# Optimization experiments

Measured on AMD Instinct MI355X. Metric: run time of the kernel, lower is better.

The kernel has to match this reference:

```python
import jax, jax.numpy as jnp
import numpy as np

L, D, H, DFF, A, S = 8, 1024, 16, 4096, 4096, 66
T = S + 1  # 67 after pool token
DK = D // H
EPS = 1e-5


def _pos_enc(t, d):
    pos = np.arange(t, dtype=np.float32)[:, None]
    div = np.exp(np.arange(0, d, 2, dtype=np.float32) * (-np.log(10000.0) / d))
    pe = np.zeros((t, d), dtype=np.float32)
    pe[:, 0::2] = np.sin(pos * div)
    pe[:, 1::2] = np.cos(pos * div)
    return jnp.asarray(pe)


def _ln(x, g, b):
    m = jnp.mean(x, axis=-1, keepdims=True)
    v = jnp.mean(jnp.square(x - m), axis=-1, keepdims=True)
    return (x - m) * jax.lax.rsqrt(v + EPS) * g + b


def setup_inputs() -> dict:
    key = jax.random.key(0)
    ks = jax.random.split(key, 12)
    B = 256
    sc = 0.02
    return {
        "x": jax.random.randint(ks[0], (B, S), 0, A, dtype=jnp.int32),
        "emb": jax.random.normal(ks[1], (A, D), jnp.float32) * sc,
        "pool": jax.random.normal(ks[2], (D,), jnp.float32) * sc,
        "Wq": jax.random.normal(ks[3], (L, D, D), jnp.float32) * sc,
        "Wk": jax.random.normal(ks[4], (L, D, D), jnp.float32) * sc,
        "Wv": jax.random.normal(ks[5], (L, D, D), jnp.float32) * sc,
        "Wo": jax.random.normal(ks[6], (L, D, D), jnp.float32) * sc,
        "rel_bias": jax.random.normal(ks[7], (L, H, 78, 78), jnp.float32) * sc,
        "ln1_g": jnp.ones((L, D), jnp.float32),
        "ln1_b": jnp.zeros((L, D), jnp.float32),
        "ln2_g": jnp.ones((L, D), jnp.float32),
        "ln2_b": jnp.zeros((L, D), jnp.float32),
        "W1": jax.random.normal(ks[8], (L, D, DFF), jnp.float32) * sc,
        "b1": jnp.zeros((L, DFF), jnp.float32),
        "W2": jax.random.normal(ks[9], (L, DFF, D), jnp.float32) * sc,
        "b2": jnp.zeros((L, D), jnp.float32),
        "Wout": jax.random.normal(ks[10], (D, A), jnp.float32) * sc,
        "bout": jnp.zeros((A,), jnp.float32),
    }


def reference(x, emb, pool, Wq, Wk, Wv, Wo, rel_bias, ln1_g, ln1_b, ln2_g, ln2_b,
              W1, b1, W2, b2, Wout, bout):
    B = x.shape[0]
    h = emb[x] * jnp.sqrt(jnp.float32(D))            # (B, S, D)
    h = jnp.concatenate([jnp.broadcast_to(pool, (B, 1, D)), h], axis=1)  # (B, T, D)
    h = h + _pos_enc(T, D)[None]
    scale = 1.0 / jnp.sqrt(jnp.float32(DK))
    for i in range(L):
        q = (h @ Wq[i]).reshape(B, T, H, DK)
        k = (h @ Wk[i]).reshape(B, T, H, DK)
        v = (h @ Wv[i]).reshape(B, T, H, DK)
        scores = jnp.einsum("bqhd,bkhd->bhqk", q, k) * scale + rel_bias[i][:, :T, :T]
        attn = jax.nn.softmax(scores, axis=-1)
        ctx = jnp.einsum("bhqk,bkhd->bqhd", attn, v).reshape(B, T, D)
        h = _ln(h + ctx @ Wo[i], ln1_g[i], ln1_b[i])
        f = jax.nn.gelu(h @ W1[i] + b1[i], approximate=False) @ W2[i] + b2[i]
        h = _ln(h + f, ln2_g[i], ln2_b[i])
    return h[:, 0, :] @ Wout + bout  # (B, A)
```

## Files before the change

### kernel.cpp

```cpp
#include <hip/hip_runtime.h>
#include <math.h>

typedef unsigned short u16;
typedef __attribute__((ext_vector_type(8))) short short8;
typedef __attribute__((ext_vector_type(4))) float f32x4;

#define LAYERS 8
#define D 1024
#define NH 16
#define DKH 64
#define DFF 4096
#define SEQ 66
#define TT 67
#define BATCH 256
#define ROWS (BATCH*TT)
#define VOCAB 4096
#define TP 80
#define KP 96
#define QS 3072

__device__ __forceinline__ float bf2f(u16 v){
  unsigned int u = ((unsigned int)v) << 16;
  return __builtin_bit_cast(float, u);
}
__device__ __forceinline__ u16 f2bf(float f){
  unsigned int u = __builtin_bit_cast(unsigned int, f);
  u += 0x7FFFu + ((u >> 16) & 1u);
  return (u16)(u >> 16);
}
__device__ __forceinline__ void gload16(const u16* g, u16* l){
  __builtin_amdgcn_global_load_lds((const __attribute__((address_space(1))) void*)g,
                                   (__attribute__((address_space(3))) void*)l, 16, 0, 0);
}

__global__ void transpose_cast(const float* __restrict__ src, u16* __restrict__ dst,
                               int R, int C){
  __shared__ float tile[32][33];
  const int c0 = blockIdx.x * 32, r0 = blockIdx.y * 32;
  const int tx = threadIdx.x, ty = threadIdx.y;
  #pragma unroll
  for (int i = 0; i < 32; i += 8)
    tile[ty + i][tx] = src[(size_t)(r0 + ty + i) * C + (c0 + tx)];
  __syncthreads();
  #pragma unroll
  for (int i = 0; i < 32; i += 8)
    dst[(size_t)(c0 + ty + i) * R + (r0 + tx)] = f2bf(tile[tx][ty + i]);
}

__global__ void embed_kernel(const int* __restrict__ x, const float* __restrict__ emb,
                             const float* __restrict__ pool, float* __restrict__ h,
                             u16* __restrict__ hb){
  const int row = blockIdx.x;
  const int b = row / TT, t = row % TT;
  const int d0 = threadIdx.x * 4;
  float v[4];
  if (t == 0){
    const float4 p4 = *(const float4*)&pool[d0];
    v[0] = p4.x; v[1] = p4.y; v[2] = p4.z; v[3] = p4.w;
  } else {
    const int id = x[b * SEQ + (t - 1)];
    const float4 e4 = *(const float4*)&emb[(size_t)id * D + d0];
    v[0] = e4.x * 32.f; v[1] = e4.y * 32.f; v[2] = e4.z * 32.f; v[3] = e4.w * 32.f;
  }
  const float c = -logf(10000.f) / (float)D;
  float o[4];
  #pragma unroll
  for (int j = 0; j < 4; j++){
    const int d = d0 + j;
    const int p = d >> 1;
    const float freq = expf((float)(2 * p) * c);
    const float ang = (float)t * freq;
    const float pe = (d & 1) ? cosf(ang) : sinf(ang);
    o[j] = v[j] + pe;
  }
  *(float4*)&h[(size_t)row * D + d0] = make_float4(o[0], o[1], o[2], o[3]);
  const unsigned int lo = (unsigned)f2bf(o[0]) | ((unsigned)f2bf(o[1]) << 16);
  const unsigned int hi = (unsigned)f2bf(o[2]) | ((unsigned)f2bf(o[3]) << 16);
  *(uint2*)&hb[(size_t)row * D + d0] = make_uint2(lo, hi);
}

__global__ void ln_kernel(float* __restrict__ h, const float* __restrict__ res,
                          u16* __restrict__ hb, const float* __restrict__ g,
                          const float* __restrict__ bta){
  const int row = blockIdx.x;
  const int tid = threadIdx.x;
  const size_t off = (size_t)row * D + tid * 4;
  const float4 a = *(const float4*)&h[off];
  const float4 r4 = *(const float4*)&res[off];
  const float s0 = a.x + r4.x, s1 = a.y + r4.y, s2 = a.z + r4.z, s3 = a.w + r4.w;
  float sum = s0 + s1 + s2 + s3;
  float sq = s0*s0 + s1*s1 + s2*s2 + s3*s3;
  #pragma unroll
  for (int m = 32; m >= 1; m >>= 1){ sum += __shfl_xor(sum, m); sq += __shfl_xor(sq, m); }
  __shared__ float red[2][4];
  const int w = tid >> 6;
  if ((tid & 63) == 0){ red[0][w] = sum; red[1][w] = sq; }
  __syncthreads();
  sum = red[0][0] + red[0][1] + red[0][2] + red[0][3];
  sq  = red[1][0] + red[1][1] + red[1][2] + red[1][3];
  const float mean = sum * (1.f / D);
  const float var = sq * (1.f / D) - mean * mean;
  const float rs = rsqrtf(var + 1e-5f);
  const float4 gv = *(const float4*)&g[tid * 4];
  const float4 bv = *(const float4*)&bta[tid * 4];
  const float o0 = (s0 - mean) * rs * gv.x + bv.x;
  const float o1 = (s1 - mean) * rs * gv.y + bv.y;
  const float o2 = (s2 - mean) * rs * gv.z + bv.z;
  const float o3 = (s3 - mean) * rs * gv.w + bv.w;
  *(float4*)&h[off] = make_float4(o0, o1, o2, o3);
  const unsigned int lo = (unsigned)f2bf(o0) | ((unsigned)f2bf(o1) << 16);
  const unsigned int hi = (unsigned)f2bf(o2) | ((unsigned)f2bf(o3) << 16);
  *(uint2*)&hb[off] = make_uint2(lo, hi);
}

__global__ __launch_bounds__(256) void attn_kernel(const u16* __restrict__ qkv,
    const float* __restrict__ rel, u16* __restrict__ ctxb){
  __shared__ u16 Qf[8 * 81 * 8];
  __shared__ u16 Kf[8 * 81 * 8];
  __shared__ u16 Vf[12 * 65 * 8];
  __shared__ u16 Pf[12 * 81 * 8];
  __shared__ float Ss[TP][84];
  const int bh = blockIdx.x;
  const int b = bh >> 4, hh = bh & 15;
  const int tid = threadIdx.x, w = tid >> 6, l = tid & 63;
  const size_t qvbase = (size_t)(b * TT) * QS + hh * DKH;
  const size_t obase  = (size_t)(b * TT) * D + hh * DKH;

  {
    const int r0 = tid >> 4, c4 = (tid & 15) * 4;
    const int g = c4 >> 3, e = c4 & 7;
    for (int r = r0; r < TP; r += 16){
      uint2 q2 = make_uint2(0u, 0u), k2 = make_uint2(0u, 0u);
      if (r < TT){
        q2 = *(const uint2*)&qkv[qvbase + (size_t)r * QS + c4];
        k2 = *(const uint2*)&qkv[qvbase + 1024 + (size_t)r * QS + c4];
      }
      *(uint2*)&Qf[(g * 81 + r) * 8 + e] = q2;
      *(uint2*)&Kf[(g * 81 + r) * 8 + e] = k2;
    }
    for (int j = r0; j < KP; j += 16){
      u16 v4[4] = {0, 0, 0, 0};
      if (j < TT) *(uint2*)v4 = *(const uint2*)&qkv[qvbase + 2048 + (size_t)j * QS + c4];
      const int gg = j >> 3, ee = j & 7;
      #pragma unroll
      for (int d = 0; d < 4; d++)
        Vf[(gg * 65 + (c4 + d)) * 8 + ee] = v4[d];
    }
  }
  __syncthreads();

  const int fr = l & 15, gg = l >> 4;
  for (int p = w; p < 25; p += 4){
    const int rt = p / 5, ct = p % 5;
    f32x4 acc = {};
    #pragma unroll
    for (int kk = 0; kk < 2; kk++){
      const short8 a  = *(const short8*)&Qf[((kk * 4 + gg) * 81 + rt * 16 + fr) * 8];
      const short8 bf = *(const short8*)&Kf[((kk * 4 + gg) * 81 + ct * 16 + fr) * 8];
      acc = __builtin_amdgcn_mfma_f32_16x16x32_bf16(a, bf, acc, 0, 0, 0);
    }
    const int col = ct * 16 + fr;
    #pragma unroll
    for (int r = 0; r < 4; r++){
      const int row = rt * 16 + gg * 4 + r;
      float sv = -1e30f;
      if (row < TT && col < TT)
        sv = acc[r] * 0.125f + rel[((size_t)hh * 78 + row) * 78 + col];
      Ss[row][col] = sv;
    }
  }
  __syncthreads();

  for (int row = w; row < TP; row += 4){
    const float s1 = Ss[row][l];
    const float s2 = (l < 16) ? Ss[row][64 + l] : -1e30f;
    float mx = fmaxf(s1, s2);
    #pragma unroll
    for (int m = 32; m >= 1; m >>= 1) mx = fmaxf(mx, __shfl_xor(mx, m));
    const float e1 = __expf(s1 - mx);
    const float e2 = (l < 16) ? __expf(s2 - mx) : 0.f;
    float sum = e1 + e2;
    #pragma unroll
    for (int m = 32; m >= 1; m >>= 1) sum += __shfl_xor(sum, m);
    const float inv = 1.f / sum;
    Pf[((l >> 3) * 81 + row) * 8 + (l & 7)] = f2bf(e1 * inv);
    if (l < 16){
      Pf[((8  + (l >> 3)) * 81 + row) * 8 + (l & 7)] = f2bf(e2 * inv);
      Pf[((10 + (l >> 3)) * 81 + row) * 8 + (l & 7)] = 0;
    }
  }
  __syncthreads();

  for (int p = w; p < 20; p += 4){
    const int rt = p >> 2, ct = p & 3;
    f32x4 acc = {};
    #pragma unroll
    for (int kk = 0; kk < 3; kk++){
      const short8 a  = *(const short8*)&Pf[((kk * 4 + gg) * 81 + rt * 16 + fr) * 8];
      const short8 bf = *(const short8*)&Vf[((kk * 4 + gg) * 65 + ct * 16 + fr) * 8];
      acc = __builtin_amdgcn_mfma_f32_16x16x32_bf16(a, bf, acc, 0, 0, 0);
    }
    #pragma unroll
    for (int r = 0; r < 4; r++){
      const int row = rt * 16 + gg * 4 + r;
      if (row < TT)
        ctxb[obase + (size_t)row * D + ct * 16 + fr] = f2bf(acc[r]);
    }
  }
}

template<int OBF16, int BIAS, int GELU>
__global__ __launch_bounds__(256, 2) void gemm_bt(
    const u16* __restrict__ A, int lda,
    const u16* __restrict__ Bt,
    void* __restrict__ Cv, int ldc,
    const float* __restrict__ bias, int K, int nby)
{
  __shared__ u16 As[128 * 32];
  __shared__ u16 Bs[128 * 32];
  const int nwg = gridDim.x, bid = blockIdx.x;
  const int q8 = nwg >> 3, r8 = nwg & 7;
  const int xcd = bid & 7, off = bid >> 3;
  const int wg = (xcd < r8 ? xcd * (q8 + 1) : r8 * (q8 + 1) + (xcd - r8) * q8) + off;
  const int m0 = (wg / nby) * 128, n0 = (wg % nby) * 128;

  const int tid = threadIdx.x;
  const int l = tid & 63, w = tid >> 6;
  const int wr = w >> 1, wc = w & 1;
  f32x4 acc[4][4] = {};
  const int lr = l >> 2;
  const int lseg = (l & 3) * 8;
  u16* aB0 = &As[(w * 32) * 32];
  u16* aB1 = &As[(w * 32 + 16) * 32];
  u16* bB0 = &Bs[(w * 32) * 32];
  u16* bB1 = &Bs[(w * 32 + 16) * 32];
  const u16* ga0 = A + (size_t)(m0 + w * 32 + lr) * lda + lseg;
  const u16* ga1 = A + (size_t)(m0 + w * 32 + 16 + lr) * lda + lseg;
  const u16* gb0 = Bt + (size_t)(n0 + w * 32 + lr) * K + lseg;
  const u16* gb1 = Bt + (size_t)(n0 + w * 32 + 16 + lr) * K + lseg;
  const int fr = l & 15, kg = (l >> 4) * 8;
  for (int kt = 0; kt < K; kt += 32){
    __syncthreads();
    gload16(ga0 + kt, aB0);
    gload16(ga1 + kt, aB1);
    gload16(gb0 + kt, bB0);
    gload16(gb1 + kt, bB1);
    __syncthreads();
    short8 af[4], bf[4];
    #pragma unroll
    for (int i = 0; i < 4; i++){
      af[i] = *(const short8*)&As[(wr * 64 + i * 16 + fr) * 32 + kg];
      bf[i] = *(const short8*)&Bs[(wc * 64 + i * 16 + fr) * 32 + kg];
    }
    #pragma unroll
    for (int i = 0; i < 4; i++)
      #pragma unroll
      for (int j = 0; j < 4; j++)
        acc[i][j] = __builtin_amdgcn_mfma_f32_16x16x32_bf16(af[i], bf[j], acc[i][j], 0, 0, 0);
  }
  const int rg = (l >> 4) * 4;
  #pragma unroll
  for (int i = 0; i < 4; i++){
    #pragma unroll
    for (int j = 0; j < 4; j++){
      const int col = n0 + wc * 64 + j * 16 + fr;
      const float bv = BIAS ? bias[col] : 0.f;
      #pragma unroll
      for (int r = 0; r < 4; r++){
        const int row = m0 + wr * 64 + i * 16 + rg + r;
        float xv = acc[i][j][r] + bv;
        if (GELU) xv = 0.5f * xv * (1.f + erff(xv * 0.70710678118f));
        if (OBF16) ((u16*)Cv)[(size_t)row * ldc + col] = f2bf(xv);
        else       ((float*)Cv)[(size_t)row * ldc + col] = xv;
      }
    }
  }
}

extern "C" void kernel_launch(void* const* d_in, const int* in_sizes, int n_in,
                              void* d_out, int out_size, void* d_ws, size_t ws_size,
                              hipStream_t stream) {
  const int*   x       = (const int*)  d_in[0];
  const float* emb     = (const float*)d_in[1];
  const float* pool    = (const float*)d_in[2];
  const float* Wq      = (const float*)d_in[3];
  const float* Wk      = (const float*)d_in[4];
  const float* Wv      = (const float*)d_in[5];
  const float* Wo      = (const float*)d_in[6];
  const float* rel     = (const float*)d_in[7];
  const float* ln1_g   = (const float*)d_in[8];
  const float* ln1_b   = (const float*)d_in[9];
  const float* ln2_g   = (const float*)d_in[10];
  const float* ln2_b   = (const float*)d_in[11];
  const float* W1      = (const float*)d_in[12];
  const float* b1      = (const float*)d_in[13];
  const float* W2      = (const float*)d_in[14];
  const float* b2      = (const float*)d_in[15];
  const float* Wout    = (const float*)d_in[16];
  const float* bout    = (const float*)d_in[17];
  float* out = (float*)d_out;

  const size_t SZ_WDD  = (size_t)D * D * 2;
  const size_t SZ_WDF  = (size_t)D * DFF * 2;
  const size_t SZ_H    = (size_t)ROWS * D * 4;
  const size_t SZ_HB   = (size_t)ROWS * D * 2;
  const size_t need = 4*SZ_WDD + 3*SZ_WDF + SZ_H + SZ_HB + 4*SZ_HB + SZ_H;
  if (ws_size < need) return;

  char* p = (char*)d_ws;
  u16* WqkvT = (u16*)p; p += 3*SZ_WDD;
  u16* WoT   = (u16*)p; p += SZ_WDD;
  u16* W1T   = (u16*)p; p += SZ_WDF;
  u16* W2T   = (u16*)p; p += SZ_WDF;
  u16* WouT  = (u16*)p; p += SZ_WDF;
  float* h   = (float*)p; p += SZ_H;
  u16* hb    = (u16*)p; p += SZ_HB;
  u16* qkv   = (u16*)p; p += 3*SZ_HB;
  u16* ctxb  = (u16*)p; p += SZ_HB;
  u16* gb    = qkv;
  float* tmp = (float*)p; p += SZ_H;

  dim3 tb(32, 8);
  transpose_cast<<<dim3(VOCAB/32, D/32), tb, 0, stream>>>(Wout, WouT, D, VOCAB);
  embed_kernel<<<ROWS, 256, 0, stream>>>(x, emb, pool, h, hb);

  const int MB = ROWS / 128;
  for (int l = 0; l < LAYERS; ++l){
    const size_t wo = (size_t)l * D * D;
    const size_t wf = (size_t)l * D * DFF;
    transpose_cast<<<dim3(D/32,   D/32),   tb, 0, stream>>>(Wq + wo, WqkvT,         D, D);
    transpose_cast<<<dim3(D/32,   D/32),   tb, 0, stream>>>(Wk + wo, WqkvT + D*D,   D, D);
    transpose_cast<<<dim3(D/32,   D/32),   tb, 0, stream>>>(Wv + wo, WqkvT + 2*D*D, D, D);
    transpose_cast<<<dim3(D/32,   D/32),   tb, 0, stream>>>(Wo + wo, WoT, D, D);
    transpose_cast<<<dim3(DFF/32, D/32),   tb, 0, stream>>>(W1 + wf, W1T, D, DFF);
    transpose_cast<<<dim3(D/32,   DFF/32), tb, 0, stream>>>(W2 + wf, W2T, DFF, D);

    gemm_bt<1,0,0><<<MB * (QS/128),  256, 0, stream>>>(hb, D, WqkvT, qkv, QS, nullptr, D, QS/128);
    attn_kernel<<<BATCH*NH, 256, 0, stream>>>(qkv, rel + (size_t)l*NH*78*78, ctxb);
    gemm_bt<0,0,0><<<MB * (D/128),   256, 0, stream>>>(ctxb, D, WoT, tmp, D, nullptr, D, D/128);
    ln_kernel<<<ROWS, 256, 0, stream>>>(h, tmp, hb, ln1_g + l*D, ln1_b + l*D);
    gemm_bt<1,1,1><<<MB * (DFF/128), 256, 0, stream>>>(hb, D, W1T, gb, DFF, b1 + l*DFF, D, DFF/128);
    gemm_bt<0,1,0><<<MB * (D/128),   256, 0, stream>>>(gb, DFF, W2T, tmp, D, b2 + l*D, DFF, D/128);
    ln_kernel<<<ROWS, 256, 0, stream>>>(h, tmp, hb, ln2_g + l*D, ln2_b + l*D);
  }
  gemm_bt<0,1,0><<<(BATCH/128) * (VOCAB/128), 256, 0, stream>>>(
      hb, TT * D, WouT, out, VOCAB, bout, D, VOCAB/128);
}
```

Baseline: 7.013 ms.

## Double-buffer GEMM LDS tiles, merge weight transposes, store residual in bf16

The GEMM now keeps two LDS buffers and issues the global-to-LDS loads for the next K tile before running the MFMAs on the current one, so there is one barrier per iteration instead of two and load latency can overlap compute. The six per-layer weight transpose launches are merged into a single kernel. The Wo and W2 GEMM outputs feeding layer norm are written as bf16 instead of fp32, which halves that traffic but loses some precision in the residual add. Doubling LDS per block may limit occupancy.

Measured after the change: 6.656 ms. 1.05x faster.

```diff
diff --git a/kernel.cpp b/kernel.cpp
--- a/kernel.cpp
+++ b/kernel.cpp
@@ -33,18 +33,43 @@
                                    (__attribute__((address_space(3))) void*)l, 16, 0, 0);
 }
 
+__device__ __forceinline__ void tc_tile(const float* __restrict__ src, u16* __restrict__ dst,
+                                        int R, int C, int bx, int by, int tx, int ty){
+  __shared__ float tile[32][33];
+  const int c0 = bx * 32, r0 = by * 32;
+  #pragma unroll
+  for (int i = 0; i < 32; i += 8)
+    tile[ty + i][tx] = src[(size_t)(r0 + ty + i) * C + (c0 + tx)];
+  __syncthreads();
+  #pragma unroll
+  for (int i = 0; i < 32; i += 8)
+    dst[(size_t)(c0 + ty + i) * R + (r0 + tx)] = f2bf(tile[tx][ty + i]);
+}
+
+__global__ void transpose6(const float* __restrict__ Wq, const float* __restrict__ Wk,
+                           const float* __restrict__ Wv, const float* __restrict__ Wo,
+                           const float* __restrict__ W1, const float* __restrict__ W2,
+                           u16* __restrict__ WqkvT, u16* __restrict__ WoT,
+                           u16* __restrict__ W1T, u16* __restrict__ W2T){
+  const int tx = threadIdx.x, ty = threadIdx.y;
+  int b = blockIdx.x;
+  if (b < 4096){
+    const int which = b >> 10, idx = b & 1023;
+    const float* s = which == 0 ? Wq : which == 1 ? Wk : which == 2 ? Wv : Wo;
+    u16* d = which == 3 ? WoT : WqkvT + which * D * D;
+    tc_tile(s, d, D, D, idx & 31, idx >> 5, tx, ty);
+  } else if (b < 8192){
+    const int idx = b - 4096;
+    tc_tile(W1, W1T, D, DFF, idx & 127, idx >> 7, tx, ty);
+  } else {
+    const int idx = b - 8192;
+    tc_tile(W2, W2T, DFF, D, idx & 31, idx >> 5, tx, ty);
+  }
+}
+
 __global__ void transpose_cast(const float* __restrict__ src, u16* __restrict__ dst,
                                int R, int C){
-  __shared__ float tile[32][33];
-  const int c0 = blockIdx.x * 32, r0 = blockIdx.y * 32;
-  const int tx = threadIdx.x, ty = threadIdx.y;
-  #pragma unroll
-  for (int i = 0; i < 32; i += 8)
-    tile[ty + i][tx] = src[(size_t)(r0 + ty + i) * C + (c0 + tx)];
-  __syncthreads();
-  #pragma unroll
-  for (int i = 0; i < 32; i += 8)
-    dst[(size_t)(c0 + ty + i) * R + (r0 + tx)] = f2bf(tile[tx][ty + i]);
+  tc_tile(src, dst, R, C, blockIdx.x, blockIdx.y, threadIdx.x, threadIdx.y);
 }
 
 __global__ void embed_kernel(const int* __restrict__ x, const float* __restrict__ emb,
@@ -79,15 +104,18 @@
   *(uint2*)&hb[(size_t)row * D + d0] = make_uint2(lo, hi);
 }
 
-__global__ void ln_kernel(float* __restrict__ h, const float* __restrict__ res,
+__global__ void ln_kernel(float* __restrict__ h, const u16* __restrict__ res,
                           u16* __restrict__ hb, const float* __restrict__ g,
                           const float* __restrict__ bta){
   const int row = blockIdx.x;
   const int tid = threadIdx.x;
   const size_t off = (size_t)row * D + tid * 4;
   const float4 a = *(const float4*)&h[off];
-  const float4 r4 = *(const float4*)&res[off];
-  const float s0 = a.x + r4.x, s1 = a.y + r4.y, s2 = a.z + r4.z, s3 = a.w + r4.w;
+  const uint2 r2 = *(const uint2*)&res[off];
+  const float s0 = a.x + bf2f((u16)(r2.x & 0xffff));
+  const float s1 = a.y + bf2f((u16)(r2.x >> 16));
+  const float s2 = a.z + bf2f((u16)(r2.y & 0xffff));
+  const float s3 = a.w + bf2f((u16)(r2.y >> 16));
   float sum = s0 + s1 + s2 + s3;
   float sq = s0*s0 + s1*s1 + s2*s2 + s3*s3;
   #pragma unroll
@@ -216,8 +244,8 @@
     void* __restrict__ Cv, int ldc,
     const float* __restrict__ bias, int K, int nby)
 {
-  __shared__ u16 As[128 * 32];
-  __shared__ u16 Bs[128 * 32];
+  __shared__ u16 As[2][128 * 32];
+  __shared__ u16 Bs[2][128 * 32];
   const int nwg = gridDim.x, bid = blockIdx.x;
   const int q8 = nwg >> 3, r8 = nwg & 7;
   const int xcd = bid & 7, off = bid >> 3;
@@ -230,34 +258,42 @@
   f32x4 acc[4][4] = {};
   const int lr = l >> 2;
   const int lseg = (l & 3) * 8;
-  u16* aB0 = &As[(w * 32) * 32];
-  u16* aB1 = &As[(w * 32 + 16) * 32];
-  u16* bB0 = &Bs[(w * 32) * 32];
-  u16* bB1 = &Bs[(w * 32 + 16) * 32];
   const u16* ga0 = A + (size_t)(m0 + w * 32 + lr) * lda + lseg;
   const u16* ga1 = A + (size_t)(m0 + w * 32 + 16 + lr) * lda + lseg;
   const u16* gb0 = Bt + (size_t)(n0 + w * 32 + lr) * K + lseg;
   const u16* gb1 = Bt + (size_t)(n0 + w * 32 + 16 + lr) * K + lseg;
   const int fr = l & 15, kg = (l >> 4) * 8;
-  for (int kt = 0; kt < K; kt += 32){
-    __syncthreads();
-    gload16(ga0 + kt, aB0);
-    gload16(ga1 + kt, aB1);
-    gload16(gb0 + kt, bB0);
-    gload16(gb1 + kt, bB1);
-    __syncthreads();
+
+#define STAGE(sel, kc) do { \
+    gload16(ga0 + (kc), &As[sel][(w * 32) * 32]); \
+    gload16(ga1 + (kc), &As[sel][(w * 32 + 16) * 32]); \
+    gload16(gb0 + (kc), &Bs[sel][(w * 32) * 32]); \
+    gload16(gb1 + (kc), &Bs[sel][(w * 32 + 16) * 32]); \
+  } while (0)
+
+  const int nkt = K >> 5;
+  STAGE(0, 0);
+  __syncthreads();
+  int cur = 0;
+  #pragma unroll 1
+  for (int kt = 0; kt < nkt; ++kt){
+    if (kt + 1 < nkt) STAGE(cur ^ 1, (kt + 1) * 32);
     short8 af[4], bf[4];
     #pragma unroll
     for (int i = 0; i < 4; i++){
-      af[i] = *(const short8*)&As[(wr * 64 + i * 16 + fr) * 32 + kg];
-      bf[i] = *(const short8*)&Bs[(wc * 64 + i * 16 + fr) * 32 + kg];
+      af[i] = *(const short8*)&As[cur][(wr * 64 + i * 16 + fr) * 32 + kg];
+      bf[i] = *(const short8*)&Bs[cur][(wc * 64 + i * 16 + fr) * 32 + kg];
     }
     #pragma unroll
     for (int i = 0; i < 4; i++)
       #pragma unroll
       for (int j = 0; j < 4; j++)
         acc[i][j] = __builtin_amdgcn_mfma_f32_16x16x32_bf16(af[i], bf[j], acc[i][j], 0, 0, 0);
-  }
+    __syncthreads();
+    cur ^= 1;
+  }
+#undef STAGE
+
   const int rg = (l >> 4) * 4;
   #pragma unroll
   for (int i = 0; i < 4; i++){
@@ -304,7 +340,7 @@
   const size_t SZ_WDF  = (size_t)D * DFF * 2;
   const size_t SZ_H    = (size_t)ROWS * D * 4;
   const size_t SZ_HB   = (size_t)ROWS * D * 2;
-  const size_t need = 4*SZ_WDD + 3*SZ_WDF + SZ_H + SZ_HB + 4*SZ_HB + SZ_H;
+  const size_t need = 4*SZ_WDD + 3*SZ_WDF + SZ_H + 6*SZ_HB;
   if (ws_size < need) return;
 
   char* p = (char*)d_ws;
@@ -318,7 +354,7 @@
   u16* qkv   = (u16*)p; p += 3*SZ_HB;
   u16* ctxb  = (u16*)p; p += SZ_HB;
   u16* gb    = qkv;
-  float* tmp = (float*)p; p += SZ_H;
+  u16* tmpb  = (u16*)p; p += SZ_HB;
 
   dim3 tb(32, 8);
   transpose_cast<<<dim3(VOCAB/32, D/32), tb, 0, stream>>>(Wout, WouT, D, VOCAB);
@@ -328,20 +364,16 @@
   for (int l = 0; l < LAYERS; ++l){
     const size_t wo = (size_t)l * D * D;
     const size_t wf = (size_t)l * D * DFF;
-    transpose_cast<<<dim3(D/32,   D/32),   tb, 0, stream>>>(Wq + wo, WqkvT,         D, D);
-    transpose_cast<<<dim3(D/32,   D/32),   tb, 0, stream>>>(Wk + wo, WqkvT + D*D,   D, D);
-    transpose_cast<<<dim3(D/32,   D/32),   tb, 0, stream>>>(Wv + wo, WqkvT + 2*D*D, D, D);
-    transpose_cast<<<dim3(D/32,   D/32),   tb, 0, stream>>>(Wo + wo, WoT, D, D);
-    transpose_cast<<<dim3(DFF/32, D/32),   tb, 0, stream>>>(W1 + wf, W1T, D, DFF);
-    transpose_cast<<<dim3(D/32,   DFF/32), tb, 0, stream>>>(W2 + wf, W2T, DFF, D);
+    transpose6<<<12288, tb, 0, stream>>>(Wq + wo, Wk + wo, Wv + wo, Wo + wo,
+                                         W1 + wf, W2 + wf, WqkvT, WoT, W1T, W2T);
 
     gemm_bt<1,0,0><<<MB * (QS/128),  256, 0, stream>>>(hb, D, WqkvT, qkv, QS, nullptr, D, QS/128);
     attn_kernel<<<BATCH*NH, 256, 0, stream>>>(qkv, rel + (size_t)l*NH*78*78, ctxb);
-    gemm_bt<0,0,0><<<MB * (D/128),   256, 0, stream>>>(ctxb, D, WoT, tmp, D, nullptr, D, D/128);
-    ln_kernel<<<ROWS, 256, 0, stream>>>(h, tmp, hb, ln1_g + l*D, ln1_b + l*D);
+    gemm_bt<1,0,0><<<MB * (D/128),   256, 0, stream>>>(ctxb, D, WoT, tmpb, D, nullptr, D, D/128);
+    ln_kernel<<<ROWS, 256, 0, stream>>>(h, tmpb, hb, ln1_g + l*D, ln1_b + l*D);
     gemm_bt<1,1,1><<<MB * (DFF/128), 256, 0, stream>>>(hb, D, W1T, gb, DFF, b1 + l*DFF, D, DFF/128);
-    gemm_bt<0,1,0><<<MB * (D/128),   256, 0, stream>>>(gb, DFF, W2T, tmp, D, b2 + l*D, DFF, D/128);
-    ln_kernel<<<ROWS, 256, 0, stream>>>(h, tmp, hb, ln2_g + l*D, ln2_b + l*D);
+    gemm_bt<1,1,0><<<MB * (D/128),   256, 0, stream>>>(gb, DFF, W2T, tmpb, D, b2 + l*D, DFF, D/128);
+    ln_kernel<<<ROWS, 256, 0, stream>>>(h, tmpb, hb, ln2_g + l*D, ln2_b + l*D);
   }
   gemm_bt<0,1,0><<<(BATCH/128) * (VOCAB/128), 256, 0, stream>>>(
       hb, TT * D, WouT, out, VOCAB, bout, D, VOCAB/128);
```
